# Kernel optimization log

Measured on AMD Instinct MI355X. Metric: run time of the kernel, lower is better.

Reference implementation:

```python
import jax, jax.numpy as jnp
import numpy as np

T_CONST = 0.1

def _hardtanh(w):
    # F.hardtanh(w, min_val=1e-10, max_val=1)
    return jnp.clip(w, 1e-10, 1.0)

def _forward(inp, hn, w_str2str, w_str2snr, w_m12m1, w_m12str, w_thal2m1,
             w_m12thal, w_thal2str, w_str2stn, w_stn2snr, w_snr2thal,
             str2str_fixed, inp_weight, mean_w, mean_b, std_w, std_b, hid_dim):
    H = hid_dim
    H5 = 5 * H
    Z = jnp.zeros((H, H), dtype=inp.dtype)
    n_inhib = int(0.3 * H)

    # Diagonal 'D' matrices realized as column scalings (D is diagonal)
    m12m1_d = jnp.concatenate([jnp.ones((H - n_inhib,)), -jnp.ones((n_inhib,))])

    # Block masks
    str2str_mask = jnp.zeros((H, H))
    m12str_mask = jnp.concatenate([jnp.ones((H, H - n_inhib)), jnp.zeros((H, n_inhib))], axis=1)
    str2stn_mask = jnp.concatenate([jnp.zeros((H, H // 2)), jnp.ones((H, H // 2))], axis=1)
    str2snr_mask = jnp.concatenate([jnp.ones((H, H // 2)), jnp.zeros((H, H // 2))], axis=1)

    # Region masks over the full 5H state
    thal_mask = jnp.concatenate([jnp.zeros((3 * H,)), jnp.ones((H,)), jnp.zeros((H,))])
    m1_mask = jnp.zeros((H5,))  # cat(zeros(4H), zeros(H)) in the source

    # Effective recurrent blocks (str2str_D = stn2snr_D = snr2thal_D = str2snr_D = -I)
    str2str_rec = -(str2str_mask * _hardtanh(w_str2str) + str2str_fixed)
    m12m1_rec = _hardtanh(w_m12m1) * m12m1_d[None, :]
    m12str_rec = m12str_mask * _hardtanh(w_m12str)
    str2snr_rec = -(str2snr_mask * _hardtanh(w_str2snr))
    thal2m1_rec = _hardtanh(w_thal2m1)
    m12thal_rec = _hardtanh(w_m12thal)
    thal2str_rec = _hardtanh(w_thal2str)
    str2stn_rec = str2stn_mask * _hardtanh(w_str2stn)
    stn2snr_rec = -_hardtanh(w_str2stn)  # NOTE: source uses str2stn weight here (faithful to original)
    snr2thal_rec = -_hardtanh(w_snr2thal)

    W_rec = jnp.concatenate([
        jnp.concatenate([str2str_rec, Z, Z, thal2str_rec, m12str_rec], axis=1),
        jnp.concatenate([str2stn_rec, Z, Z, Z, Z], axis=1),
        jnp.concatenate([str2snr_rec, stn2snr_rec, Z, Z, Z], axis=1),
        jnp.concatenate([Z, Z, snr2thal_rec, Z, m12thal_rec], axis=1),
        jnp.concatenate([Z, Z, Z, thal2m1_rec, m12m1_rec], axis=1),
    ], axis=0)  # [5H, 5H]

    # Precompute masked input drive for all timesteps: [T, B, 5H]
    u = jnp.einsum('bti,ih->tbh', inp, _hardtanh(inp_weight)) * thal_mask

    W_rec_T = W_rec.T

    def step(h, u_t):
        # (W_rec @ h.T).T == h @ W_rec.T
        h_new = jax.nn.relu((1.0 - T_CONST) * h + T_CONST * (h @ W_rec_T + u_t))
        return h_new, h_new

    _, hs = jax.lax.scan(step, hn[0], u)  # hs: [T, B, 5H]
    rnn_out = jnp.transpose(hs, (1, 0, 2))  # [B, T, 5H]
    hn_last = rnn_out[:, -1, :][None]  # [1, B, 5H]

    masked = rnn_out * m1_mask
    mean_out = masked @ mean_w + mean_b
    std_out = jnp.clip(masked @ std_w + std_b, -5.0, 10.0)
    return mean_out, std_out, rnn_out, hn_last


def setup_inputs() -> dict:
    H, B, T, I, A = 256, 64, 512, 4, 1
    H5 = 5 * H
    key = jax.random.key(0)
    ks = jax.random.split(key, 20)
    u01 = lambda k, shape, s: jax.random.uniform(k, shape, dtype=jnp.float32) * s
    inputs = {
        'inp': jax.random.uniform(ks[0], (B, T, I), dtype=jnp.float32),
        'hn': jnp.zeros((1, B, H5), dtype=jnp.float32),
        'w_str2str': u01(ks[1], (H, H), 0.01),
        'w_str2snr': u01(ks[2], (H, H), 0.01),
        'w_m12m1': u01(ks[3], (H, H), 0.01),
        'w_m12str': u01(ks[4], (H, H), 0.01),
        'w_thal2m1': u01(ks[5], (H, H), 0.01),
        'w_m12thal': u01(ks[6], (H, H), 0.01),
        'w_thal2str': u01(ks[7], (H, H), 0.01),
        'w_str2stn': u01(ks[8], (H, H), 0.01),
        'w_stn2snr': u01(ks[9], (H, H), 0.01),
        'w_snr2thal': u01(ks[10], (H, H), 0.01),
        'inp_weight': u01(ks[12], (I, H5), 0.1),
        'mean_w': jax.random.normal(ks[13], (H5, A), dtype=jnp.float32) * 0.02,
        'mean_b': jnp.zeros((A,), dtype=jnp.float32),
        'std_w': jax.random.normal(ks[14], (H5, A), dtype=jnp.float32) * 0.02,
        'std_b': jnp.zeros((A,), dtype=jnp.float32),
        'hid_dim': H,
    }
    keep = jax.random.bernoulli(ks[11], 0.15, (H, H)).astype(jnp.float32)
    inputs['str2str_fixed'] = u01(ks[15], (H, H), 0.01) * keep
    return inputs


def reference(inp, hn, w_str2str, w_str2snr, w_m12m1, w_m12str, w_thal2m1,
              w_m12thal, w_thal2str, w_str2stn, w_stn2snr, w_snr2thal,
              str2str_fixed, inp_weight, mean_w, mean_b, std_w, std_b, hid_dim):
    return _forward(inp, hn, w_str2str, w_str2snr, w_m12m1, w_m12str, w_thal2m1,
                    w_m12thal, w_thal2str, w_str2stn, w_stn2snr, w_snr2thal,
                    str2str_fixed, inp_weight, mean_w, mean_b, std_w, std_b, hid_dim)
```

## Files before the change

### kernel.cpp

```cpp
#include <hip/hip_runtime.h>

typedef unsigned short u16;
typedef __bf16 v8bf __attribute__((ext_vector_type(8)));
typedef float f32x4 __attribute__((ext_vector_type(4)));
typedef u16 u16x4 __attribute__((ext_vector_type(4)));

#define H5 1280
#define TT 512
#define NBLK 80
#define SPL 81920

#define OFF_W0 0
#define OFF_W1 3276800
#define OFF_W2 6553600
#define OFF_HS 9830400
#define OFF_WIN 10813440

#define MFMA(a, b, c) __builtin_amdgcn_mfma_f32_16x16x32_bf16(a, b, c, 0, 0, 0)

__device__ __forceinline__ float htanh_(float x) {
  return fminf(fmaxf(x, 1e-10f), 1.0f);
}
__device__ __forceinline__ u16 f2b(float f) {
  unsigned u = __float_as_uint(f);
  return (u16)((u + 0x7fffu + ((u >> 16) & 1u)) >> 16);
}
__device__ __forceinline__ float b2f(u16 b) {
  return __uint_as_float(((unsigned)b) << 16);
}

__global__ void build_w(const float* __restrict__ w_str2snr, const float* __restrict__ w_m12m1,
                        const float* __restrict__ w_m12str, const float* __restrict__ w_thal2m1,
                        const float* __restrict__ w_m12thal, const float* __restrict__ w_thal2str,
                        const float* __restrict__ w_str2stn, const float* __restrict__ w_snr2thal,
                        const float* __restrict__ fixedw, u16* __restrict__ W0,
                        u16* __restrict__ W1, u16* __restrict__ W2) {
  int idx = blockIdx.x * 256 + threadIdx.x;
  if (idx >= H5 * H5) return;
  int j = idx / H5, k = idx - j * H5;
  int jr = j >> 8, kr = k >> 8, kk = k & 255;
  int o = (j & 255) * 256 + kk;
  float w = 0.0f;
  if (jr == 0) {
    if (kr == 0) w = -fixedw[o];
    else if (kr == 3) w = htanh_(w_thal2str[o]);
    else if (kr == 4) w = (kk < 180) ? htanh_(w_m12str[o]) : 0.0f;
  } else if (jr == 1) {
    if (kr == 0) w = (kk >= 128) ? htanh_(w_str2stn[o]) : 0.0f;
  } else if (jr == 2) {
    if (kr == 0) w = (kk < 128) ? -htanh_(w_str2snr[o]) : 0.0f;
    else if (kr == 1) w = -htanh_(w_str2stn[o]);
  } else if (jr == 3) {
    if (kr == 2) w = -htanh_(w_snr2thal[o]);
    else if (kr == 4) w = htanh_(w_m12thal[o]);
  } else {
    if (kr == 3) w = htanh_(w_thal2m1[o]);
    else if (kr == 4) w = (kk < 180) ? htanh_(w_m12m1[o]) : -htanh_(w_m12m1[o]);
  }
  u16 c0 = f2b(w);  float r1 = w - b2f(c0);
  u16 c1 = f2b(r1); float r2 = r1 - b2f(c1);
  u16 c2 = f2b(r2);
  W0[idx] = c0; W1[idx] = c1; W2[idx] = c2;
}

__global__ void build_misc(const float* __restrict__ hn, const float* __restrict__ inp_weight,
                           const float* __restrict__ mean_b, const float* __restrict__ std_b,
                           float* __restrict__ out, u16* __restrict__ hs, float* __restrict__ Win) {
  int gid = blockIdx.x * 256 + threadIdx.x;
  if (gid < 65536) {
    out[gid] = (gid < 32768) ? mean_b[0] : fminf(10.0f, fmaxf(-5.0f, std_b[0]));
  } else if (gid < 65536 + SPL) {
    int i = gid - 65536;
    float v = hn[i];
    u16 c0 = f2b(v);  float r1 = v - b2f(c0);
    u16 c1 = f2b(r1); float r2 = r1 - b2f(c1);
    u16 c2 = f2b(r2);
    hs[i] = c0; hs[SPL + i] = c1; hs[2 * SPL + i] = c2;
  } else if (gid < 65536 + SPL + 1024) {
    int i = gid - 65536 - SPL;
    Win[i] = htanh_(inp_weight[(i >> 8) * H5 + 768 + (i & 255)]);
  }
}

template <int R> struct RC;
template <> struct RC<0> { static constexpr int kb[3] = {0, 768, 1024}; static constexpr int nch[3] = {8, 8, 8}; };
template <> struct RC<1> { static constexpr int kb[3] = {128, 0, 0};    static constexpr int nch[3] = {4, 0, 0}; };
template <> struct RC<2> { static constexpr int kb[3] = {0, 256, 0};    static constexpr int nch[3] = {4, 8, 0}; };
template <> struct RC<3> { static constexpr int kb[3] = {512, 1024, 0}; static constexpr int nch[3] = {8, 8, 0}; };
template <> struct RC<4> { static constexpr int kb[3] = {768, 1024, 0}; static constexpr int nch[3] = {8, 8, 0}; };

template <int R>
__device__ __forceinline__ f32x4 do_mm(const u16* __restrict__ hs_r, int b, int lk,
                                       const u16* __restrict__ w0r, const u16* __restrict__ w1r,
                                       const u16* __restrict__ w2r) {
  f32x4 A00 = {0.f, 0.f, 0.f, 0.f}, A01 = {0.f, 0.f, 0.f, 0.f}, A02 = {0.f, 0.f, 0.f, 0.f};
  f32x4 A10 = {0.f, 0.f, 0.f, 0.f}, A11 = {0.f, 0.f, 0.f, 0.f}, A20 = {0.f, 0.f, 0.f, 0.f};
#pragma unroll
  for (int q = 0; q < 3; ++q) {
    if (RC<R>::nch[q] > 0) {
      const int kbq = RC<R>::kb[q];
      const u16* hb = hs_r + (long)b * H5 + kbq + lk;
#pragma unroll
      for (int c = 0; c < RC<R>::nch[q]; ++c) {
        v8bf h0 = *(const v8bf*)(hb + c * 32);
        v8bf h1 = *(const v8bf*)(hb + SPL + c * 32);
        v8bf h2 = *(const v8bf*)(hb + 2 * SPL + c * 32);
        v8bf a0 = *(const v8bf*)(w0r + kbq + c * 32);
        v8bf a1 = *(const v8bf*)(w1r + kbq + c * 32);
        v8bf a2 = *(const v8bf*)(w2r + kbq + c * 32);
        A00 = MFMA(a0, h0, A00);
        A01 = MFMA(a0, h1, A01);
        A02 = MFMA(a0, h2, A02);
        A10 = MFMA(a1, h0, A10);
        A11 = MFMA(a1, h1, A11);
        A20 = MFMA(a2, h0, A20);
      }
    }
  }
  f32x4 acc;
#pragma unroll
  for (int rr = 0; rr < 4; ++rr)
    acc[rr] = ((A00[rr] + A10[rr]) + (A01[rr] + A11[rr])) + (A02[rr] + A20[rr]);
  return acc;
}

template <int R>
__device__ void step_one(int t, int j0, int b, int lr, int hi, int lk,
                         const float* __restrict__ inp_b, const float* __restrict__ hn,
                         const u16* __restrict__ W0, const u16* __restrict__ W1,
                         const u16* __restrict__ W2, u16* __restrict__ hs,
                         float* __restrict__ rnn, float* __restrict__ rnn_b,
                         float* __restrict__ hn_last, const float* __restrict__ Win) {
  const long jrow = (long)(j0 + lr) * H5 + lk;
  const u16* hs_r = hs + (t & 1) * (3 * SPL);
  u16* hs_w = hs + ((t & 1) ^ 1) * (3 * SPL);

  f32x4 acc = do_mm<R>(hs_r, b, lk, W0 + jrow, W1 + jrow, W2 + jrow);

  if constexpr (R == 3) {
    float winreg[4][4];
#pragma unroll
    for (int i = 0; i < 4; ++i)
#pragma unroll
      for (int rr = 0; rr < 4; ++rr)
        winreg[i][rr] = Win[i * 256 + (j0 - 768) + hi * 4 + rr];
    const float* ip = inp_b + t * 4;
    float i0 = ip[0], i1 = ip[1], i2 = ip[2], i3 = ip[3];
#pragma unroll
    for (int rr = 0; rr < 4; ++rr)
      acc[rr] += i0 * winreg[0][rr] + i1 * winreg[1][rr] + i2 * winreg[2][rr] + i3 * winreg[3][rr];
  }

  f32x4 hprev;
  {
    const float* hp = (t == 0) ? (hn + (long)b * H5 + j0 + hi * 4)
                               : (rnn + ((long)b * TT + (t - 1)) * H5 + j0 + hi * 4);
#pragma unroll
    for (int rr = 0; rr < 4; ++rr) hprev[rr] = hp[rr];
  }
  f32x4 hnew;
#pragma unroll
  for (int rr = 0; rr < 4; ++rr)
    hnew[rr] = fmaxf(0.0f, 0.9f * hprev[rr] + 0.1f * acc[rr]);

  *(f32x4*)(rnn_b + (long)t * H5 + j0 + hi * 4) = hnew;
  if (t < TT - 1) {
    u16x4 s0, s1, s2;
#pragma unroll
    for (int rr = 0; rr < 4; ++rr) {
      float v = hnew[rr];
      u16 c0 = f2b(v);  float r1 = v - b2f(c0);
      u16 c1 = f2b(r1); float r2 = r1 - b2f(c1);
      s0[rr] = c0; s1[rr] = c1; s2[rr] = f2b(r2);
    }
    u16* hw = hs_w + (long)b * H5 + j0 + hi * 4;
    *(u16x4*)(hw) = s0;
    *(u16x4*)(hw + SPL) = s1;
    *(u16x4*)(hw + 2 * SPL) = s2;
  } else {
    float* hl = hn_last + (long)b * H5 + j0 + hi * 4;
#pragma unroll
    for (int rr = 0; rr < 4; ++rr) hl[rr] = hnew[rr];
  }
}

__global__ void __launch_bounds__(256, 1)
rnn_step(const float* __restrict__ inp, const float* __restrict__ hn,
         const u16* __restrict__ W0, const u16* __restrict__ W1, const u16* __restrict__ W2,
         u16* __restrict__ hs, float* __restrict__ rnn, float* __restrict__ hn_last,
         const float* __restrict__ Win, int t) {
  const int lane = threadIdx.x & 63;
  const int lr = lane & 15, hi = lane >> 4, lk = hi * 8;
  const int g = blockIdx.x & 3;
  const int i = blockIdx.x >> 2;
  const int w = threadIdx.x >> 6;
  const int jt = i * 4 + w;
  const int j0 = jt << 4;
  const int b = (g << 4) + lr;
  float* rnn_b = rnn + (long)b * TT * H5;
  const float* inp_b = inp + (long)b * TT * 4;
  switch (i >> 2) {
    case 0: step_one<0>(t, j0, b, lr, hi, lk, inp_b, hn, W0, W1, W2, hs, rnn, rnn_b, hn_last, Win); break;
    case 1: step_one<1>(t, j0, b, lr, hi, lk, inp_b, hn, W0, W1, W2, hs, rnn, rnn_b, hn_last, Win); break;
    case 2: step_one<2>(t, j0, b, lr, hi, lk, inp_b, hn, W0, W1, W2, hs, rnn, rnn_b, hn_last, Win); break;
    case 3: step_one<3>(t, j0, b, lr, hi, lk, inp_b, hn, W0, W1, W2, hs, rnn, rnn_b, hn_last, Win); break;
    default: step_one<4>(t, j0, b, lr, hi, lk, inp_b, hn, W0, W1, W2, hs, rnn, rnn_b, hn_last, Win); break;
  }
}

extern "C" void kernel_launch(void* const* d_in, const int* in_sizes, int n_in,
                              void* d_out, int out_size, void* d_ws, size_t ws_size,
                              hipStream_t stream) {
  const float* inp        = (const float*)d_in[0];
  const float* hn         = (const float*)d_in[1];
  const float* w_str2snr  = (const float*)d_in[3];
  const float* w_m12m1    = (const float*)d_in[4];
  const float* w_m12str   = (const float*)d_in[5];
  const float* w_thal2m1  = (const float*)d_in[6];
  const float* w_m12thal  = (const float*)d_in[7];
  const float* w_thal2str = (const float*)d_in[8];
  const float* w_str2stn  = (const float*)d_in[9];
  const float* w_snr2thal = (const float*)d_in[11];
  const float* inp_weight = (const float*)d_in[12];
  const float* mean_b     = (const float*)d_in[14];
  const float* std_b      = (const float*)d_in[16];
  const float* fixedw     = (const float*)d_in[18];

  char* ws = (char*)d_ws;
  u16* W0 = (u16*)(ws + OFF_W0);
  u16* W1 = (u16*)(ws + OFF_W1);
  u16* W2 = (u16*)(ws + OFF_W2);
  u16* hsb = (u16*)(ws + OFF_HS);
  float* Win = (float*)(ws + OFF_WIN);

  float* out = (float*)d_out;
  float* rnn = out + 65536;
  float* hnl = out + 65536 + 41943040;

  build_w<<<6400, 256, 0, stream>>>(w_str2snr, w_m12m1, w_m12str, w_thal2m1, w_m12thal,
                                    w_thal2str, w_str2stn, w_snr2thal, fixedw, W0, W1, W2);
  build_misc<<<581, 256, 0, stream>>>(hn, inp_weight, mean_b, std_b, out, hsb, Win);

  for (int t = 0; t < TT; ++t)
    rnn_step<<<NBLK, 256, 0, stream>>>(inp, hn, W0, W1, W2, hsb, rnn, hnl, Win, t);
}
```

Measured before the change: 9.301 ms.

## Replace per-timestep launches with persistent cooperative kernel using flag barriers

Replaces the 512 per-timestep kernel launches with a single cooperative persistent kernel. The blocks synchronise within each group of 8 batch columns through global flag polling, so there are no full-device barriers. Each block stages the bf16-split hidden state into LDS and computes two row tiles per wave. It keeps the previous hidden state in registers instead of reloading it from the output. The launch overhead per step is traded for spin-wait synchronisation, and correctness now depends on co-residency and cache-bypass (sc1) memory ordering. A fallback to the multi-launch path is kept.

```diff
diff --git a/kernel.cpp b/kernel.cpp
--- a/kernel.cpp
+++ b/kernel.cpp
@@ -1,9 +1,13 @@
 #include <hip/hip_runtime.h>
 
 typedef unsigned short u16;
+typedef unsigned long long u64;
+typedef unsigned u32;
 typedef __bf16 v8bf __attribute__((ext_vector_type(8)));
 typedef float f32x4 __attribute__((ext_vector_type(4)));
 typedef u16 u16x4 __attribute__((ext_vector_type(4)));
+typedef u32 u32x4 __attribute__((ext_vector_type(4)));
+typedef u32 u32x2 __attribute__((ext_vector_type(2)));
 
 #define H5 1280
 #define TT 512
@@ -15,6 +19,7 @@
 #define OFF_W2 6553600
 #define OFF_HS 9830400
 #define OFF_WIN 10813440
+#define OFF_CNT 10817536
 
 #define MFMA(a, b, c) __builtin_amdgcn_mfma_f32_16x16x32_bf16(a, b, c, 0, 0, 0)
 
@@ -27,6 +32,13 @@
 }
 __device__ __forceinline__ float b2f(u16 b) {
   return __uint_as_float(((unsigned)b) << 16);
+}
+__device__ __forceinline__ u32 umin_(u32 a, u32 b) { return a < b ? a : b; }
+
+__device__ __forceinline__ void st8_sc1(u16* p, u16x4 v) {
+  union { u16x4 s; u64 q; } u;
+  u.s = v;
+  asm volatile("global_store_dwordx2 %0, %1, off sc1" :: "v"(p), "v"(u.q) : "memory");
 }
 
 __global__ void build_w(const float* __restrict__ w_str2snr, const float* __restrict__ w_m12m1,
@@ -90,97 +102,365 @@
 template <> struct RC<4> { static constexpr int kb[3] = {768, 1024, 0}; static constexpr int nch[3] = {8, 8, 0}; };
 
 template <int R>
-__device__ __forceinline__ f32x4 do_mm(const u16* __restrict__ hs_r, int b, int lk,
-                                       const u16* __restrict__ w0r, const u16* __restrict__ w1r,
-                                       const u16* __restrict__ w2r) {
-  f32x4 A00 = {0.f, 0.f, 0.f, 0.f}, A01 = {0.f, 0.f, 0.f, 0.f}, A02 = {0.f, 0.f, 0.f, 0.f};
-  f32x4 A10 = {0.f, 0.f, 0.f, 0.f}, A11 = {0.f, 0.f, 0.f, 0.f}, A20 = {0.f, 0.f, 0.f, 0.f};
+__device__ __forceinline__ void stage_h(const u16* __restrict__ hs_r, int bcol0,
+                                        u16* __restrict__ sm) {
+  v8bf regs[9];
+  int n = 0;
+#pragma unroll
+  for (int q = 0; q < 3; ++q) {
+    if (RC<R>::nch[q] > 0) {
+      const int span8 = RC<R>::nch[q] * 4;
+      const int units = span8 * 24;
+      const int rounds = (units + 255) / 256;
+#pragma unroll
+      for (int r = 0; r < rounds; ++r) {
+        int u = threadIdx.x + r * 256;
+        if (u < units) {
+          int kunit = u & (span8 - 1);
+          int sc = u / span8;
+          int split = sc >> 3, col = sc & 7;
+          const u16* gp = hs_r + split * SPL + (long)(bcol0 + col) * H5 +
+                          RC<R>::kb[q] + kunit * 8;
+          asm volatile("global_load_dwordx4 %0, %1, off sc1"
+                       : "=v"(regs[n]) : "v"(gp) : "memory");
+        }
+        ++n;
+      }
+    }
+  }
+  asm volatile("s_waitcnt vmcnt(0)" ::: "memory");
+  __builtin_amdgcn_sched_barrier(0);
+  n = 0;
+  int base = 0;
+#pragma unroll
+  for (int q = 0; q < 3; ++q) {
+    if (RC<R>::nch[q] > 0) {
+      const int span8 = RC<R>::nch[q] * 4;
+      const int colstride = RC<R>::nch[q] * 32 + 8;
+      const int units = span8 * 24;
+      const int rounds = (units + 255) / 256;
+#pragma unroll
+      for (int r = 0; r < rounds; ++r) {
+        int u = threadIdx.x + r * 256;
+        if (u < units) {
+          int kunit = u & (span8 - 1);
+          int sc = u / span8;
+          *(v8bf*)(sm + base + sc * colstride + kunit * 8) = regs[n];
+        }
+        ++n;
+      }
+      base += 24 * colstride;
+    }
+  }
+}
+
+template <int R>
+__device__ __forceinline__ void mm_lds(const u16* __restrict__ sm, int lk, int col,
+                                       const u16* __restrict__ W0, const u16* __restrict__ W1,
+                                       const u16* __restrict__ W2, long jrowA, long jrowB,
+                                       f32x4 (&out)[2]) {
+  f32x4 acc[2][6];
+#pragma unroll
+  for (int t = 0; t < 2; ++t)
+#pragma unroll
+    for (int s = 0; s < 6; ++s) acc[t][s] = {0.f, 0.f, 0.f, 0.f};
+  int base = 0;
 #pragma unroll
   for (int q = 0; q < 3; ++q) {
     if (RC<R>::nch[q] > 0) {
       const int kbq = RC<R>::kb[q];
-      const u16* hb = hs_r + (long)b * H5 + kbq + lk;
+      const int colstride = RC<R>::nch[q] * 32 + 8;
 #pragma unroll
       for (int c = 0; c < RC<R>::nch[q]; ++c) {
-        v8bf h0 = *(const v8bf*)(hb + c * 32);
-        v8bf h1 = *(const v8bf*)(hb + SPL + c * 32);
-        v8bf h2 = *(const v8bf*)(hb + 2 * SPL + c * 32);
-        v8bf a0 = *(const v8bf*)(w0r + kbq + c * 32);
-        v8bf a1 = *(const v8bf*)(w1r + kbq + c * 32);
-        v8bf a2 = *(const v8bf*)(w2r + kbq + c * 32);
-        A00 = MFMA(a0, h0, A00);
-        A01 = MFMA(a0, h1, A01);
-        A02 = MFMA(a0, h2, A02);
-        A10 = MFMA(a1, h0, A10);
-        A11 = MFMA(a1, h1, A11);
-        A20 = MFMA(a2, h0, A20);
-      }
-    }
-  }
-  f32x4 acc;
-#pragma unroll
-  for (int rr = 0; rr < 4; ++rr)
-    acc[rr] = ((A00[rr] + A10[rr]) + (A01[rr] + A11[rr])) + (A02[rr] + A20[rr]);
-  return acc;
+        v8bf B0 = *(const v8bf*)(sm + base + (0 * 8 + col) * colstride + c * 32 + lk);
+        v8bf B1 = *(const v8bf*)(sm + base + (1 * 8 + col) * colstride + c * 32 + lk);
+        v8bf B2 = *(const v8bf*)(sm + base + (2 * 8 + col) * colstride + c * 32 + lk);
+        long oA = jrowA + kbq + c * 32, oB = jrowB + kbq + c * 32;
+        v8bf a0 = *(const v8bf*)(W0 + oA);
+        v8bf a1 = *(const v8bf*)(W1 + oA);
+        v8bf a2 = *(const v8bf*)(W2 + oA);
+        v8bf b0 = *(const v8bf*)(W0 + oB);
+        v8bf b1 = *(const v8bf*)(W1 + oB);
+        v8bf b2 = *(const v8bf*)(W2 + oB);
+        acc[0][0] = MFMA(a0, B0, acc[0][0]);
+        acc[1][0] = MFMA(b0, B0, acc[1][0]);
+        acc[0][1] = MFMA(a0, B1, acc[0][1]);
+        acc[1][1] = MFMA(b0, B1, acc[1][1]);
+        acc[0][2] = MFMA(a0, B2, acc[0][2]);
+        acc[1][2] = MFMA(b0, B2, acc[1][2]);
+        acc[0][3] = MFMA(a1, B0, acc[0][3]);
+        acc[1][3] = MFMA(b1, B0, acc[1][3]);
+        acc[0][4] = MFMA(a1, B1, acc[0][4]);
+        acc[1][4] = MFMA(b1, B1, acc[1][4]);
+        acc[0][5] = MFMA(a2, B0, acc[0][5]);
+        acc[1][5] = MFMA(b2, B0, acc[1][5]);
+      }
+      base += 24 * colstride;
+    }
+  }
+#pragma unroll
+  for (int t = 0; t < 2; ++t)
+#pragma unroll
+    for (int rr = 0; rr < 4; ++rr)
+      out[t][rr] = ((acc[t][0][rr] + acc[t][3][rr]) + (acc[t][1][rr] + acc[t][4][rr])) +
+                   (acc[t][2][rr] + acc[t][5][rr]);
 }
 
 template <int R>
-__device__ void step_one(int t, int j0, int b, int lr, int hi, int lk,
+__device__ void pers_loop(int j0, int bcol, bool act, int hi, int lk, int lr, int bcol0,
+                          const float* __restrict__ inp_b, const float* __restrict__ hn,
+                          const u16* __restrict__ W0, const u16* __restrict__ W1,
+                          const u16* __restrict__ W2, u16* __restrict__ hs,
+                          float* __restrict__ rnn_b, float* __restrict__ hn_last,
+                          const float* __restrict__ Win, u32* __restrict__ flags, int slot,
+                          u16* __restrict__ sm) {
+  const long jrowA = (long)(j0 + lr) * H5 + lk;
+  const long jrowB = (long)(j0 + 16 + lr) * H5 + lk;
+  const int col = lr & 7;
+
+  float wA[4][4], wB[4][4];
+  if constexpr (R == 3) {
+#pragma unroll
+    for (int i = 0; i < 4; ++i)
+#pragma unroll
+      for (int rr = 0; rr < 4; ++rr) {
+        wA[i][rr] = Win[i * 256 + (j0 - 768) + hi * 4 + rr];
+        wB[i][rr] = Win[i * 256 + (j0 - 768 + 16) + hi * 4 + rr];
+      }
+  }
+
+  f32x4 hpA, hpB;
+  {
+    const float* ha = hn + (long)bcol * H5 + j0 + hi * 4;
+#pragma unroll
+    for (int rr = 0; rr < 4; ++rr) { hpA[rr] = ha[rr]; hpB[rr] = ha[16 + rr]; }
+  }
+
+  for (int t = 0; t < TT; ++t) {
+    const u16* hs_r = hs + (t & 1) * (3 * SPL);
+    u16* hs_w = hs + ((t & 1) ^ 1) * (3 * SPL);
+
+    stage_h<R>(hs_r, bcol0, sm);
+    __syncthreads();
+
+    f32x4 o[2];
+    mm_lds<R>(sm, lk, col, W0, W1, W2, jrowA, jrowB, o);
+
+    if constexpr (R == 3) {
+      const float* ip = inp_b + t * 4;
+      float i0 = ip[0], i1 = ip[1], i2 = ip[2], i3 = ip[3];
+#pragma unroll
+      for (int rr = 0; rr < 4; ++rr) {
+        o[0][rr] += i0 * wA[0][rr] + i1 * wA[1][rr] + i2 * wA[2][rr] + i3 * wA[3][rr];
+        o[1][rr] += i0 * wB[0][rr] + i1 * wB[1][rr] + i2 * wB[2][rr] + i3 * wB[3][rr];
+      }
+    }
+
+    f32x4 hA, hB;
+#pragma unroll
+    for (int rr = 0; rr < 4; ++rr) {
+      hA[rr] = fmaxf(0.0f, 0.9f * hpA[rr] + 0.1f * o[0][rr]);
+      hB[rr] = fmaxf(0.0f, 0.9f * hpB[rr] + 0.1f * o[1][rr]);
+    }
+    hpA = hA; hpB = hB;
+
+    if (act) {
+      float* rp = rnn_b + (long)t * H5 + j0 + hi * 4;
+      *(f32x4*)rp = hA;
+      *(f32x4*)(rp + 16) = hB;
+    }
+
+    if (t < TT - 1) {
+      if (act) {
+        u16x4 sA0, sA1, sA2, sB0, sB1, sB2;
+#pragma unroll
+        for (int rr = 0; rr < 4; ++rr) {
+          float v = hA[rr];
+          u16 c0 = f2b(v);  float r1 = v - b2f(c0);
+          u16 c1 = f2b(r1); float r2 = r1 - b2f(c1);
+          sA0[rr] = c0; sA1[rr] = c1; sA2[rr] = f2b(r2);
+          v = hB[rr];
+          c0 = f2b(v);  r1 = v - b2f(c0);
+          c1 = f2b(r1); r2 = r1 - b2f(c1);
+          sB0[rr] = c0; sB1[rr] = c1; sB2[rr] = f2b(r2);
+        }
+        u16* hw = hs_w + (long)bcol * H5 + j0 + hi * 4;
+        st8_sc1(hw, sA0);
+        st8_sc1(hw + SPL, sA1);
+        st8_sc1(hw + 2 * SPL, sA2);
+        st8_sc1(hw + 16, sB0);
+        st8_sc1(hw + 16 + SPL, sB1);
+        st8_sc1(hw + 16 + 2 * SPL, sB2);
+      }
+      asm volatile("s_waitcnt vmcnt(0)" ::: "memory");
+      __syncthreads();
+      if (threadIdx.x == 0) {
+        u32 tv = (u32)(t + 1);
+        u32* myf = flags + slot;
+        asm volatile("global_store_dword %0, %1, off sc1" :: "v"(myf), "v"(tv) : "memory");
+        for (;;) {
+          u32x4 f0, f1; u32x2 f2;
+          asm volatile("global_load_dwordx4 %0, %1, off sc1" : "=v"(f0) : "v"(flags) : "memory");
+          asm volatile("global_load_dwordx4 %0, %1, off sc1" : "=v"(f1) : "v"(flags + 4) : "memory");
+          asm volatile("global_load_dwordx2 %0, %1, off sc1" : "=v"(f2) : "v"(flags + 8) : "memory");
+          asm volatile("s_waitcnt vmcnt(0)" ::: "memory");
+          u32 m = umin_(umin_(umin_(f0[0], f0[1]), umin_(f0[2], f0[3])),
+                        umin_(umin_(f1[0], f1[1]), umin_(f1[2], f1[3])));
+          m = umin_(m, umin_(f2[0], f2[1]));
+          if (m >= tv) break;
+          __builtin_amdgcn_s_sleep(1);
+        }
+      }
+      __syncthreads();
+    } else if (act) {
+      float* hl = hn_last + (long)bcol * H5 + j0 + hi * 4;
+      *(f32x4*)hl = hA;
+      *(f32x4*)(hl + 16) = hB;
+    }
+  }
+}
+
+__global__ void __launch_bounds__(256, 1)
+rnn_pers(const float* __restrict__ inp, const float* __restrict__ hn,
+         const u16* __restrict__ W0, const u16* __restrict__ W1, const u16* __restrict__ W2,
+         u16* __restrict__ hs, float* __restrict__ rnn, float* __restrict__ hn_last,
+         const float* __restrict__ Win, u32* __restrict__ cnt) {
+  __shared__ u16 smh[19008];
+  const int tid = threadIdx.x, bx = blockIdx.x;
+  const int g = bx & 7, slot = bx >> 3;
+  const int lane = tid & 63, w = tid >> 6;
+  const int lr = lane & 15, hi = lane >> 4, lk = hi * 8;
+  const int bcol0 = g * 8;
+  const int bcol = bcol0 + (lr & 7);
+  const bool act = lr < 8;
+  const int j0 = slot * 128 + w * 32;
+  u32* flags = cnt + 128 + g * 32;
+  float* rnn_b = rnn + (long)bcol * TT * H5;
+  const float* inp_b = inp + (long)bcol * TT * 4;
+  switch (slot >> 1) {
+    case 0: pers_loop<0>(j0, bcol, act, hi, lk, lr, bcol0, inp_b, hn, W0, W1, W2, hs, rnn_b, hn_last, Win, flags, slot, smh); break;
+    case 1: pers_loop<1>(j0, bcol, act, hi, lk, lr, bcol0, inp_b, hn, W0, W1, W2, hs, rnn_b, hn_last, Win, flags, slot, smh); break;
+    case 2: pers_loop<2>(j0, bcol, act, hi, lk, lr, bcol0, inp_b, hn, W0, W1, W2, hs, rnn_b, hn_last, Win, flags, slot, smh); break;
+    case 3: pers_loop<3>(j0, bcol, act, hi, lk, lr, bcol0, inp_b, hn, W0, W1, W2, hs, rnn_b, hn_last, Win, flags, slot, smh); break;
+    default: pers_loop<4>(j0, bcol, act, hi, lk, lr, bcol0, inp_b, hn, W0, W1, W2, hs, rnn_b, hn_last, Win, flags, slot, smh); break;
+  }
+}
+
+template <int R>
+__device__ void step_one(int t, int j0, int bcol, bool act, int hi, int lk, int lr,
                          const float* __restrict__ inp_b, const float* __restrict__ hn,
                          const u16* __restrict__ W0, const u16* __restrict__ W1,
                          const u16* __restrict__ W2, u16* __restrict__ hs,
                          float* __restrict__ rnn, float* __restrict__ rnn_b,
                          float* __restrict__ hn_last, const float* __restrict__ Win) {
-  const long jrow = (long)(j0 + lr) * H5 + lk;
+  const long jrowA = (long)(j0 + lr) * H5 + lk;
+  const long jrowB = (long)(j0 + 16 + lr) * H5 + lk;
   const u16* hs_r = hs + (t & 1) * (3 * SPL);
   u16* hs_w = hs + ((t & 1) ^ 1) * (3 * SPL);
 
-  f32x4 acc = do_mm<R>(hs_r, b, lk, W0 + jrow, W1 + jrow, W2 + jrow);
+  f32x4 acc[2][6];
+#pragma unroll
+  for (int tt = 0; tt < 2; ++tt)
+#pragma unroll
+    for (int s = 0; s < 6; ++s) acc[tt][s] = {0.f, 0.f, 0.f, 0.f};
+#pragma unroll
+  for (int q = 0; q < 3; ++q) {
+    if (RC<R>::nch[q] > 0) {
+      const int kbq = RC<R>::kb[q];
+      const u16* hb = hs_r + (long)bcol * H5 + kbq + lk;
+#pragma unroll
+      for (int c = 0; c < RC<R>::nch[q]; ++c) {
+        v8bf B0 = *(const v8bf*)(hb + c * 32);
+        v8bf B1 = *(const v8bf*)(hb + SPL + c * 32);
+        v8bf B2 = *(const v8bf*)(hb + 2 * SPL + c * 32);
+        long oA = jrowA + kbq + c * 32, oB = jrowB + kbq + c * 32;
+        v8bf a0 = *(const v8bf*)(W0 + oA);
+        v8bf a1 = *(const v8bf*)(W1 + oA);
+        v8bf a2 = *(const v8bf*)(W2 + oA);
+        v8bf b0 = *(const v8bf*)(W0 + oB);
+        v8bf b1 = *(const v8bf*)(W1 + oB);
+        v8bf b2 = *(const v8bf*)(W2 + oB);
+        acc[0][0] = MFMA(a0, B0, acc[0][0]);
+        acc[1][0] = MFMA(b0, B0, acc[1][0]);
+        acc[0][1] = MFMA(a0, B1, acc[0][1]);
+        acc[1][1] = MFMA(b0, B1, acc[1][1]);
+        acc[0][2] = MFMA(a0, B2, acc[0][2]);
+        acc[1][2] = MFMA(b0, B2, acc[1][2]);
+        acc[0][3] = MFMA(a1, B0, acc[0][3]);
+        acc[1][3] = MFMA(b1, B0, acc[1][3]);
+        acc[0][4] = MFMA(a1, B1, acc[0][4]);
+        acc[1][4] = MFMA(b1, B1, acc[1][4]);
+        acc[0][5] = MFMA(a2, B0, acc[0][5]);
+        acc[1][5] = MFMA(b2, B0, acc[1][5]);
+      }
+    }
+  }
+  f32x4 o[2];
+#pragma unroll
+  for (int tt = 0; tt < 2; ++tt)
+#pragma unroll
+    for (int rr = 0; rr < 4; ++rr)
+      o[tt][rr] = ((acc[tt][0][rr] + acc[tt][3][rr]) + (acc[tt][1][rr] + acc[tt][4][rr])) +
+                  (acc[tt][2][rr] + acc[tt][5][rr]);
 
   if constexpr (R == 3) {
-    float winreg[4][4];
-#pragma unroll
-    for (int i = 0; i < 4; ++i)
-#pragma unroll
-      for (int rr = 0; rr < 4; ++rr)
-        winreg[i][rr] = Win[i * 256 + (j0 - 768) + hi * 4 + rr];
     const float* ip = inp_b + t * 4;
     float i0 = ip[0], i1 = ip[1], i2 = ip[2], i3 = ip[3];
 #pragma unroll
-    for (int rr = 0; rr < 4; ++rr)
-      acc[rr] += i0 * winreg[0][rr] + i1 * winreg[1][rr] + i2 * winreg[2][rr] + i3 * winreg[3][rr];
-  }
-
-  f32x4 hprev;
+    for (int rr = 0; rr < 4; ++rr) {
+      o[0][rr] += i0 * Win[0 * 256 + (j0 - 768) + hi * 4 + rr] +
+                  i1 * Win[1 * 256 + (j0 - 768) + hi * 4 + rr] +
+                  i2 * Win[2 * 256 + (j0 - 768) + hi * 4 + rr] +
+                  i3 * Win[3 * 256 + (j0 - 768) + hi * 4 + rr];
+      o[1][rr] += i0 * Win[0 * 256 + (j0 - 768 + 16) + hi * 4 + rr] +
+                  i1 * Win[1 * 256 + (j0 - 768 + 16) + hi * 4 + rr] +
+                  i2 * Win[2 * 256 + (j0 - 768 + 16) + hi * 4 + rr] +
+                  i3 * Win[3 * 256 + (j0 - 768 + 16) + hi * 4 + rr];
+    }
+  }
+
+  f32x4 hpA, hpB;
   {
-    const float* hp = (t == 0) ? (hn + (long)b * H5 + j0 + hi * 4)
-                               : (rnn + ((long)b * TT + (t - 1)) * H5 + j0 + hi * 4);
-#pragma unroll
-    for (int rr = 0; rr < 4; ++rr) hprev[rr] = hp[rr];
-  }
-  f32x4 hnew;
-#pragma unroll
-  for (int rr = 0; rr < 4; ++rr)
-    hnew[rr] = fmaxf(0.0f, 0.9f * hprev[rr] + 0.1f * acc[rr]);
-
-  *(f32x4*)(rnn_b + (long)t * H5 + j0 + hi * 4) = hnew;
-  if (t < TT - 1) {
-    u16x4 s0, s1, s2;
-#pragma unroll
-    for (int rr = 0; rr < 4; ++rr) {
-      float v = hnew[rr];
-      u16 c0 = f2b(v);  float r1 = v - b2f(c0);
-      u16 c1 = f2b(r1); float r2 = r1 - b2f(c1);
-      s0[rr] = c0; s1[rr] = c1; s2[rr] = f2b(r2);
-    }
-    u16* hw = hs_w + (long)b * H5 + j0 + hi * 4;
-    *(u16x4*)(hw) = s0;
-    *(u16x4*)(hw + SPL) = s1;
-    *(u16x4*)(hw + 2 * SPL) = s2;
-  } else {
-    float* hl = hn_last + (long)b * H5 + j0 + hi * 4;
-#pragma unroll
-    for (int rr = 0; rr < 4; ++rr) hl[rr] = hnew[rr];
+    const float* ha = (t == 0) ? (hn + (long)bcol * H5 + j0 + hi * 4)
+                               : (rnn + ((long)bcol * TT + (t - 1)) * H5 + j0 + hi * 4);
+#pragma unroll
+    for (int rr = 0; rr < 4; ++rr) { hpA[rr] = ha[rr]; hpB[rr] = ha[16 + rr]; }
+  }
+  f32x4 hA, hB;
+#pragma unroll
+  for (int rr = 0; rr < 4; ++rr) {
+    hA[rr] = fmaxf(0.0f, 0.9f * hpA[rr] + 0.1f * o[0][rr]);
+    hB[rr] = fmaxf(0.0f, 0.9f * hpB[rr] + 0.1f * o[1][rr]);
+  }
+  if (act) {
+    float* rp = rnn_b + (long)t * H5 + j0 + hi * 4;
+    *(f32x4*)rp = hA;
+    *(f32x4*)(rp + 16) = hB;
+    if (t < TT - 1) {
+      u16x4 sA0, sA1, sA2, sB0, sB1, sB2;
+#pragma unroll
+      for (int rr = 0; rr < 4; ++rr) {
+        float v = hA[rr];
+        u16 c0 = f2b(v);  float r1 = v - b2f(c0);
+        u16 c1 = f2b(r1); float r2 = r1 - b2f(c1);
+        sA0[rr] = c0; sA1[rr] = c1; sA2[rr] = f2b(r2);
+        v = hB[rr];
+        c0 = f2b(v);  r1 = v - b2f(c0);
+        c1 = f2b(r1); r2 = r1 - b2f(c1);
+        sB0[rr] = c0; sB1[rr] = c1; sB2[rr] = f2b(r2);
+      }
+      u16* hw = hs_w + (long)bcol * H5 + j0 + hi * 4;
+      *(u64*)hw = *(u64*)&sA0;
+      *(u64*)(hw + SPL) = *(u64*)&sA1;
+      *(u64*)(hw + 2 * SPL) = *(u64*)&sA2;
+      *(u64*)(hw + 16) = *(u64*)&sB0;
+      *(u64*)(hw + 16 + SPL) = *(u64*)&sB1;
+      *(u64*)(hw + 16 + 2 * SPL) = *(u64*)&sB2;
+    } else {
+      float* hl = hn_last + (long)bcol * H5 + j0 + hi * 4;
+      *(f32x4*)hl = hA;
+      *(f32x4*)(hl + 16) = hB;
+    }
   }
 }
 
@@ -189,22 +469,21 @@
          const u16* __restrict__ W0, const u16* __restrict__ W1, const u16* __restrict__ W2,
          u16* __restrict__ hs, float* __restrict__ rnn, float* __restrict__ hn_last,
          const float* __restrict__ Win, int t) {
-  const int lane = threadIdx.x & 63;
+  const int tid = threadIdx.x, bx = blockIdx.x;
+  const int g = bx & 7, slot = bx >> 3;
+  const int lane = tid & 63, w = tid >> 6;
   const int lr = lane & 15, hi = lane >> 4, lk = hi * 8;
-  const int g = blockIdx.x & 3;
-  const int i = blockIdx.x >> 2;
-  const int w = threadIdx.x >> 6;
-  const int jt = i * 4 + w;
-  const int j0 = jt << 4;
-  const int b = (g << 4) + lr;
-  float* rnn_b = rnn + (long)b * TT * H5;
-  const float* inp_b = inp + (long)b * TT * 4;
-  switch (i >> 2) {
-    case 0: step_one<0>(t, j0, b, lr, hi, lk, inp_b, hn, W0, W1, W2, hs, rnn, rnn_b, hn_last, Win); break;
-    case 1: step_one<1>(t, j0, b, lr, hi, lk, inp_b, hn, W0, W1, W2, hs, rnn, rnn_b, hn_last, Win); break;
-    case 2: step_one<2>(t, j0, b, lr, hi, lk, inp_b, hn, W0, W1, W2, hs, rnn, rnn_b, hn_last, Win); break;
-    case 3: step_one<3>(t, j0, b, lr, hi, lk, inp_b, hn, W0, W1, W2, hs, rnn, rnn_b, hn_last, Win); break;
-    default: step_one<4>(t, j0, b, lr, hi, lk, inp_b, hn, W0, W1, W2, hs, rnn, rnn_b, hn_last, Win); break;
+  const int bcol = g * 8 + (lr & 7);
+  const bool act = lr < 8;
+  const int j0 = slot * 128 + w * 32;
+  float* rnn_b = rnn + (long)bcol * TT * H5;
+  const float* inp_b = inp + (long)bcol * TT * 4;
+  switch (slot >> 1) {
+    case 0: step_one<0>(t, j0, bcol, act, hi, lk, lr, inp_b, hn, W0, W1, W2, hs, rnn, rnn_b, hn_last, Win); break;
+    case 1: step_one<1>(t, j0, bcol, act, hi, lk, lr, inp_b, hn, W0, W1, W2, hs, rnn, rnn_b, hn_last, Win); break;
+    case 2: step_one<2>(t, j0, bcol, act, hi, lk, lr, inp_b, hn, W0, W1, W2, hs, rnn, rnn_b, hn_last, Win); break;
+    case 3: step_one<3>(t, j0, bcol, act, hi, lk, lr, inp_b, hn, W0, W1, W2, hs, rnn, rnn_b, hn_last, Win); break;
+    default: step_one<4>(t, j0, bcol, act, hi, lk, lr, inp_b, hn, W0, W1, W2, hs, rnn, rnn_b, hn_last, Win); break;
   }
 }
 
@@ -232,6 +511,7 @@
   u16* W2 = (u16*)(ws + OFF_W2);
   u16* hsb = (u16*)(ws + OFF_HS);
   float* Win = (float*)(ws + OFF_WIN);
+  u32* cnt = (u32*)(ws + OFF_CNT);
 
   float* out = (float*)d_out;
   float* rnn = out + 65536;
@@ -241,6 +521,17 @@
                                     w_thal2str, w_str2stn, w_snr2thal, fixedw, W0, W1, W2);
   build_misc<<<581, 256, 0, stream>>>(hn, inp_weight, mean_b, std_b, out, hsb, Win);
 
-  for (int t = 0; t < TT; ++t)
-    rnn_step<<<NBLK, 256, 0, stream>>>(inp, hn, W0, W1, W2, hsb, rnn, hnl, Win, t);
-}
+  bool coop_ok = (ws_size >= (size_t)OFF_CNT + 2048);
+  hipError_t e = hipErrorUnknown;
+  if (coop_ok) {
+    hipMemsetAsync(cnt, 0, 1536, stream);
+    void* args[] = {(void*)&inp, (void*)&hn, (void*)&W0, (void*)&W1, (void*)&W2, (void*)&hsb,
+                    (void*)&rnn, (void*)&hnl, (void*)&Win, (void*)&cnt};
+    e = hipLaunchCooperativeKernel((const void*)rnn_pers, dim3(NBLK), dim3(256),
+                                   args, 0, stream);
+  }
+  if (e != hipSuccess) {
+    for (int t = 0; t < TT; ++t)
+      rnn_step<<<NBLK, 256, 0, stream>>>(inp, hn, W0, W1, W2, hsb, rnn, hnl, Win, t);
+  }
+}
```

Measured after the change: 10.39 ms. +11.7%, slower.
